# Kernel tuning notes

Measured on AMD Instinct MI355X. Metric: run time of the kernel, lower is better.

Reference implementation:

```python
import jax, jax.numpy as jnp
import numpy as np

CHEB_K = 3  # diffusion_steps

def setup_inputs() -> dict:
    key = jax.random.key(0)
    k1, k2, k3 = jax.random.split(key, 3)
    N, D, B, C, O, K = 2048, 16, 64, 64, 64, CHEB_K
    node_embeddings = jax.random.normal(k1, (N, D), dtype=jnp.float32)
    feat = jax.random.normal(k2, (B, N, C), dtype=jnp.float32)
    # kaiming-uniform-like init for weights_pool, zeros bias (matches reset_parameters)
    fan_in = K * C  # fan_in of [D, K, C, O] per torch convention (dims after first)
    bound = 1.0 / np.sqrt(fan_in)
    weights_pool = jax.random.uniform(k3, (D, K, C, O), dtype=jnp.float32,
                                      minval=-bound, maxval=bound)
    bias_pool = jnp.zeros((D, O), dtype=jnp.float32)
    return {"node_embeddings": node_embeddings, "feat": feat,
            "weights_pool": weights_pool, "bias_pool": bias_pool}

def reference(node_embeddings, feat, weights_pool, bias_pool):
    N = node_embeddings.shape[0]
    K = weights_pool.shape[1]
    # adaptive adjacency: softmax(relu(E E^T)) row-wise
    sim = node_embeddings @ node_embeddings.T            # [N, N]
    supports = jax.nn.softmax(jax.nn.relu(sim), axis=1)  # [N, N]
    # Chebyshev polynomial recurrence: T0=I, T1=A, Tk = 2A Tk-1 - Tk-2
    support_set = [jnp.eye(N, dtype=supports.dtype), supports]
    for _ in range(2, K):
        support_set.append(2.0 * supports @ support_set[-1] - support_set[-2])
    supports_k = jnp.stack(support_set, axis=0)          # [K, N, N]
    # node-conditioned weights and bias
    weights = jnp.einsum('nd,dkio->nkio', node_embeddings, weights_pool)  # [N,K,C,O]
    bias = node_embeddings @ bias_pool                                    # [N, O]
    # graph diffusion of features
    x_g = jnp.einsum('knm,bmc->bknc', supports_k, feat)  # [B, K, N, C]
    x_g = jnp.transpose(x_g, (0, 2, 1, 3))               # [B, N, K, C]
    # per-node batched GEMM + bias
    x_gconv = jnp.einsum('bnki,nkio->bno', x_g, weights) + bias
    return x_gconv
```

## Files before the change

kernel.cpp:

```cpp
#include <hip/hip_runtime.h>
#include <stdint.h>

#define NN 2048
#define DE 16
#define BB 64
#define CC 64
#define OO 64
#define BC 4096
#define KR 192
#define JJ 12288

using bf16x8 = __attribute__((ext_vector_type(8))) __bf16;
using f32x4  = __attribute__((ext_vector_type(4))) float;

__device__ __forceinline__ unsigned short f2bf(float f) {
  union { float f; unsigned int u; } v; v.f = f;
  unsigned int u = v.u;
  return (unsigned short)((u + 0x7FFFu + ((u >> 16) & 1u)) >> 16);
}
__device__ __forceinline__ float bf2f(unsigned short h) {
  union { unsigned int u; float f; } v; v.u = ((unsigned int)h) << 16;
  return v.f;
}
__device__ __forceinline__ void gll16(const void* g, void* l) {
  __builtin_amdgcn_global_load_lds(
      (const __attribute__((address_space(1))) unsigned int*)g,
      (__attribute__((address_space(3))) unsigned int*)l, 16, 0, 0);
}

__global__ __launch_bounds__(256) void prep(const float* __restrict__ feat,
                                            const float* __restrict__ E,
                                            const float* __restrict__ wp,
                                            const float* __restrict__ bp,
                                            unsigned short* __restrict__ Fbf,
                                            unsigned short* __restrict__ FbfT,
                                            unsigned short* __restrict__ Abf,
                                            float* __restrict__ Bias,
                                            unsigned short* __restrict__ Ebf,
                                            unsigned short* __restrict__ wpT2) {
  __shared__ float smem[64 * 65];
  const int id = blockIdx.x;
  const int t  = threadIdx.x;

  if (id < 2048) {
    float (*tile)[65] = (float (*)[65])smem;
    const int b  = id >> 5;
    const int n0 = (id & 31) * 64;
    const int tr = t >> 4, tc4 = (t & 15) * 4;
#pragma unroll
    for (int i = 0; i < 4; ++i) {
      const int r = tr + i * 16;
      const float4 v = *(const float4*)(feat + (size_t)b * (NN * CC) + (size_t)(n0 + r) * CC + tc4);
      tile[r][tc4 + 0] = v.x; tile[r][tc4 + 1] = v.y;
      tile[r][tc4 + 2] = v.z; tile[r][tc4 + 3] = v.w;
    }
    __syncthreads();
#pragma unroll
    for (int i = 0; i < 4; ++i) {
      const int r = tr + i * 16;
      const unsigned int lo = f2bf(tile[r][tc4 + 0]) | ((unsigned int)f2bf(tile[r][tc4 + 1]) << 16);
      const unsigned int hi = f2bf(tile[r][tc4 + 2]) | ((unsigned int)f2bf(tile[r][tc4 + 3]) << 16);
      *(uint2*)(Fbf + (size_t)(n0 + r) * BC + b * CC + tc4) = make_uint2(lo, hi);
    }
    const int rr = t & 63;
    const int cb = t >> 6;
#pragma unroll
    for (int i = 0; i < 16; ++i) {
      const int c = cb * 16 + i;
      FbfT[(size_t)(b * CC + c) * NN + n0 + rr] = f2bf(tile[rr][c]);
    }
  } else if (id < 4096) {
    const int n = id - 2048;
    float* en  = smem;
    float* red = smem + 16;
    if (t < 16) en[t] = E[n * 16 + t];
    __syncthreads();
    if (t < 16) Ebf[n * 16 + t] = f2bf(en[t]);
    float er[16];
#pragma unroll
    for (int d = 0; d < 16; ++d) er[d] = en[d];

    float v[8];
    float mx = 0.0f;
#pragma unroll
    for (int i = 0; i < 8; ++i) {
      const int m = t + i * 256;
      const float4* Em = (const float4*)(E + m * 16);
      const float4 a = Em[0], b = Em[1], c = Em[2], d = Em[3];
      float dot = er[0] * a.x + er[1] * a.y + er[2] * a.z + er[3] * a.w
                + er[4] * b.x + er[5] * b.y + er[6] * b.z + er[7] * b.w
                + er[8] * c.x + er[9] * c.y + er[10] * c.z + er[11] * c.w
                + er[12] * d.x + er[13] * d.y + er[14] * d.z + er[15] * d.w;
      v[i] = fmaxf(dot, 0.0f);
      mx = fmaxf(mx, v[i]);
    }
#pragma unroll
    for (int off = 32; off > 0; off >>= 1) mx = fmaxf(mx, __shfl_xor(mx, off, 64));
    const int wave = t >> 6, lane = t & 63;
    if (lane == 0) red[wave] = mx;
    __syncthreads();
    mx = fmaxf(fmaxf(red[0], red[1]), fmaxf(red[2], red[3]));
    float s = 0.0f;
#pragma unroll
    for (int i = 0; i < 8; ++i) { v[i] = __expf(v[i] - mx); s += v[i]; }
#pragma unroll
    for (int off = 32; off > 0; off >>= 1) s += __shfl_xor(s, off, 64);
    if (lane == 0) red[4 + wave] = s;
    __syncthreads();
    s = red[4] + red[5] + red[6] + red[7];
    const float inv = 1.0f / s;
#pragma unroll
    for (int i = 0; i < 8; ++i)
      Abf[(size_t)n * NN + t + i * 256] = f2bf(v[i] * inv);
    if (t < 64) {
      float bs = 0.0f;
#pragma unroll
      for (int d = 0; d < 16; ++d) bs += er[d] * bp[d * 64 + t];
      Bias[n * 64 + t] = bs;
    }
  } else {
    const int rq = id - 4096;
    for (int p = t; p < 1024; p += 256) {
      const int e0 = p * 8;
      const int d0 = e0 & 15;
      const int rem = e0 >> 4;
      const int rl = rem & 7, o = rem >> 3;
      const int r = rq * 8 + rl;
      unsigned int w[4];
#pragma unroll
      for (int u = 0; u < 4; ++u) {
        const float f0 = wp[(size_t)(d0 + 2 * u) * JJ + r * 64 + o];
        const float f1 = wp[(size_t)(d0 + 2 * u + 1) * JJ + r * 64 + o];
        w[u] = f2bf(f0) | ((unsigned int)f2bf(f1) << 16);
      }
      *(uint4*)(wpT2 + (size_t)rq * 8192 + e0) = make_uint4(w[0], w[1], w[2], w[3]);
    }
  }
}

template <int EPI, int MW>
__global__ __launch_bounds__(256, 4) void gemm_mw(const unsigned short* __restrict__ A,
                                                  const unsigned short* __restrict__ Bt,
                                                  unsigned short* __restrict__ Cnm,
                                                  unsigned short* __restrict__ Ct,
                                                  const unsigned short* __restrict__ F,
                                                  const unsigned short* __restrict__ Ebf,
                                                  const unsigned short* __restrict__ wpT2,
                                                  unsigned short* __restrict__ Wg) {
  __shared__ alignas(16) unsigned short As[128 * 64];
  __shared__ alignas(16) unsigned short Bs[64 * 64];
  const int id = blockIdx.x;
  const int t = threadIdx.x;
  const int wave = t >> 6, lane = t & 63;
  const int li = lane & 15, q = lane >> 4;

  if (MW && id >= 1024) {
    const int wid = id - 1024;
    const int bj = (wid % 96) * 128;
    const int bm = (wid / 96) * 128;
    gll16(Ebf  + (size_t)(bm + (t >> 1)) * 16 + (t & 1) * 8, &As[t * 8]);
    gll16(wpT2 + (size_t)(bj + (t >> 1)) * 16 + (t & 1) * 8, &Bs[t * 8]);
    __syncthreads();
    const int wm = (wave >> 1) * 64, wj = (wave & 1) * 64;
    const bool hiK = (q >= 2);
    const int qq = q & 1;
    bf16x8 vz;
#pragma unroll
    for (int i = 0; i < 8; ++i) vz[i] = (__bf16)0.0f;
    bf16x8 af[4], bfr[4];
#pragma unroll
    for (int r = 0; r < 4; ++r) {
      af[r] = *(const bf16x8*)&As[(wm + r * 16 + li) * 16 + qq * 8];
      if (hiK) af[r] = vz;
    }
#pragma unroll
    for (int c = 0; c < 4; ++c) {
      bfr[c] = *(const bf16x8*)&Bs[(wj + c * 16 + li) * 16 + qq * 8];
      if (hiK) bfr[c] = vz;
    }
    const int rowL = q * 4;
#pragma unroll
    for (int r = 0; r < 4; ++r) {
#pragma unroll
      for (int c = 0; c < 4; ++c) {
        f32x4 acc = (f32x4){0.f, 0.f, 0.f, 0.f};
        acc = __builtin_amdgcn_mfma_f32_16x16x32_bf16(af[r], bfr[c], acc, 0, 0, 0);
        const int gm = bm + wm + r * 16 + rowL;
        const int gj = bj + wj + c * 16 + li;
#pragma unroll
        for (int i = 0; i < 4; ++i)
          Wg[(size_t)(gm + i) * JJ + gj] = f2bf(acc[i]);
      }
    }
    return;
  }

  const int bm = (id >> 6) * 128, bn = (id & 63) * 64;
  const int wm = wave * 32;

  f32x4 acc[2][4];
#pragma unroll
  for (int r = 0; r < 2; ++r)
#pragma unroll
    for (int c = 0; c < 4; ++c) acc[r][c] = (f32x4){0.f, 0.f, 0.f, 0.f};

  const int srow = t >> 3;
  const int csw = (((t & 7) ^ ((t >> 4) & 7)) * 8);
  const unsigned short* Ap[4];
  const unsigned short* Bp[2];
#pragma unroll
  for (int i = 0; i < 4; ++i) Ap[i] = A + (size_t)(bm + srow + i * 32) * NN + csw;
#pragma unroll
  for (int i = 0; i < 2; ++i) Bp[i] = Bt + (size_t)(bn + srow + i * 32) * NN + csw;
  const int sw = (li >> 1) & 7;

  for (int k0 = 0; k0 < NN; k0 += 64) {
    __syncthreads();
#pragma unroll
    for (int i = 0; i < 4; ++i) gll16(Ap[i] + k0, &As[(t + i * 256) * 8]);
#pragma unroll
    for (int i = 0; i < 2; ++i) gll16(Bp[i] + k0, &Bs[(t + i * 256) * 8]);
    __syncthreads();
#pragma unroll
    for (int kk = 0; kk < 2; ++kk) {
      const int kc = ((kk * 4 + q) ^ sw) * 8;
      bf16x8 af[2], bfr[4];
#pragma unroll
      for (int r = 0; r < 2; ++r)
        af[r] = *(const bf16x8*)&As[(wm + r * 16 + li) * 64 + kc];
#pragma unroll
      for (int c = 0; c < 4; ++c)
        bfr[c] = *(const bf16x8*)&Bs[(c * 16 + li) * 64 + kc];
#pragma unroll
      for (int r = 0; r < 2; ++r)
#pragma unroll
        for (int c = 0; c < 4; ++c)
          acc[r][c] = __builtin_amdgcn_mfma_f32_16x16x32_bf16(af[r], bfr[c], acc[r][c], 0, 0, 0);
    }
  }

  const int rowL = q * 4;
#pragma unroll
  for (int r = 0; r < 2; ++r) {
#pragma unroll
    for (int c = 0; c < 4; ++c) {
      const int gm = bm + wm + r * 16 + rowL;
      const int gn = bn + c * 16 + li;
      const f32x4 a = acc[r][c];
      if (EPI == 1) {
#pragma unroll
        for (int i = 0; i < 4; ++i)
          Cnm[(size_t)(gm + i) * BC + gn] = f2bf(a[i]);
        const unsigned int lo = f2bf(a[0]) | ((unsigned int)f2bf(a[1]) << 16);
        const unsigned int hi = f2bf(a[2]) | ((unsigned int)f2bf(a[3]) << 16);
        *(uint2*)(Ct + (size_t)gn * NN + gm) = make_uint2(lo, hi);
      } else {
#pragma unroll
        for (int i = 0; i < 4; ++i) {
          const float g = 2.0f * a[i] - bf2f(F[(size_t)(gm + i) * BC + gn]);
          Cnm[(size_t)(gm + i) * BC + gn] = f2bf(g);
        }
      }
    }
  }
}

__global__ __launch_bounds__(256) void final_gemm(const unsigned short* __restrict__ Fbf,
                                                  const unsigned short* __restrict__ G1,
                                                  const unsigned short* __restrict__ G2,
                                                  const unsigned short* __restrict__ Wg,
                                                  const float* __restrict__ Bias,
                                                  float* __restrict__ out) {
  __shared__ alignas(16) unsigned short Xl[64 * 200];
  __shared__ alignas(16) unsigned short Wl[KR * OO];
  const int n = blockIdx.x, t = threadIdx.x;
  const unsigned short* srcs[3] = {Fbf + (size_t)n * BC, G1 + (size_t)n * BC, G2 + (size_t)n * BC};
#pragma unroll
  for (int kk = 0; kk < 3; ++kk) {
    const uint4* s = (const uint4*)srcs[kk];
    for (int p = t; p < 512; p += 256) {
      const uint4 v = s[p];
      const int j = p * 8, b = j >> 6, i = j & 63;
      *(uint4*)&Xl[b * 200 + kk * 64 + i] = v;
    }
  }
  {
    const uint4* s = (const uint4*)(Wg + (size_t)n * JJ);
    uint4* d = (uint4*)Wl;
    for (int p = t; p < 1536; p += 256) d[p] = s[p];
  }
  __syncthreads();

  const int wave = t >> 6, lane = t & 63;
  const int q = lane >> 4;
  const int brow = wave * 16 + (lane & 15);
  f32x4 acc[4];
#pragma unroll
  for (int c = 0; c < 4; ++c) acc[c] = (f32x4){0.f, 0.f, 0.f, 0.f};
#pragma unroll
  for (int kq = 0; kq < 6; ++kq) {
    const bf16x8 a = *(const bf16x8*)&Xl[brow * 200 + kq * 32 + q * 8];
#pragma unroll
    for (int c = 0; c < 4; ++c) {
      const bf16x8 b = *(const bf16x8*)&Wl[(kq * 4 + q) * 512 + (c * 16 + (lane & 15)) * 8];
      acc[c] = __builtin_amdgcn_mfma_f32_16x16x32_bf16(a, b, acc[c], 0, 0, 0);
    }
  }
  const int col = lane & 15, rbase = wave * 16 + q * 4;
#pragma unroll
  for (int c = 0; c < 4; ++c) {
    const int o = c * 16 + col;
    const float bs = Bias[n * 64 + o];
#pragma unroll
    for (int i = 0; i < 4; ++i)
      out[(size_t)(rbase + i) * (NN * OO) + (size_t)n * OO + o] = acc[c][i] + bs;
  }
}

extern "C" void kernel_launch(void* const* d_in, const int* in_sizes, int n_in,
                              void* d_out, int out_size, void* d_ws, size_t ws_size,
                              hipStream_t stream) {
  const float* E    = (const float*)d_in[0];
  const float* feat = (const float*)d_in[1];
  const float* wp   = (const float*)d_in[2];
  const float* bp   = (const float*)d_in[3];
  float* out = (float*)d_out;

  char* ws = (char*)d_ws;
  size_t off = 0;
  auto alloc = [&](size_t bytes) -> void* {
    void* p = ws + off;
    off += (bytes + 255) & ~(size_t)255;
    return p;
  };
  unsigned short* Abf  = (unsigned short*)alloc((size_t)NN * NN * 2);
  unsigned short* FbfT = (unsigned short*)alloc((size_t)BC * NN * 2);
  unsigned short* Fbf  = (unsigned short*)alloc((size_t)NN * BC * 2);
  unsigned short* G1   = (unsigned short*)alloc((size_t)NN * BC * 2);
  unsigned short* G1T  = (unsigned short*)alloc((size_t)BC * NN * 2);
  unsigned short* Wg   = (unsigned short*)alloc((size_t)NN * JJ * 2);
  float* Bias          = (float*)alloc((size_t)NN * OO * 4);
  unsigned short* Ebf  = (unsigned short*)alloc((size_t)NN * DE * 2);
  unsigned short* wpT2 = (unsigned short*)alloc((size_t)JJ * DE * 2);
  unsigned short* G2   = FbfT;

  prep<<<dim3(4120), 256, 0, stream>>>(feat, E, wp, bp, Fbf, FbfT, Abf, Bias, Ebf, wpT2);
  gemm_mw<1, 1><<<dim3(2560), 256, 0, stream>>>(Abf, FbfT, G1, G1T, nullptr, Ebf, wpT2, Wg);
  gemm_mw<2, 0><<<dim3(1024), 256, 0, stream>>>(Abf, G1T, G2, nullptr, Fbf, Ebf, wpT2, Wg);
  final_gemm<<<dim3(2048), 256, 0, stream>>>(Fbf, G1, G2, Wg, Bias, out);
}
```

Before: 223.8 us.

## Vectorize FbfT transpose, remap GEMM blocks per XCD, drop LDS in final GEMM

The prep kernel now writes the transposed bf16 feature tile with packed 4-element stores instead of scalar 2-byte stores. The Chebyshev GEMM remaps block ids so that each of the 8 XCDs works on its own pair of row panels, which should improve L2 reuse of A. Occupancy hints go from 4 to 6 blocks per SM. The weight-generation blocks move from the first diffusion GEMM to the second. final_gemm no longer stages into LDS and instead loads MFMA operands straight from global memory, removing the sync and LDS traffic at the cost of less coalesced, possibly redundant global loads.

Result: slower. 277.8 us (+24.2%).

```diff
diff --git a/kernel.cpp b/kernel.cpp
--- a/kernel.cpp
+++ b/kernel.cpp
@@ -62,12 +62,13 @@
       const unsigned int hi = f2bf(tile[r][tc4 + 2]) | ((unsigned int)f2bf(tile[r][tc4 + 3]) << 16);
       *(uint2*)(Fbf + (size_t)(n0 + r) * BC + b * CC + tc4) = make_uint2(lo, hi);
     }
-    const int rr = t & 63;
-    const int cb = t >> 6;
-#pragma unroll
-    for (int i = 0; i < 16; ++i) {
-      const int c = cb * 16 + i;
-      FbfT[(size_t)(b * CC + c) * NN + n0 + rr] = f2bf(tile[rr][c]);
+#pragma unroll
+    for (int u = 0; u < 4; ++u) {
+      const int p = t + u * 256;
+      const int c = p >> 4, n4 = (p & 15) * 4;
+      const unsigned int lo = f2bf(tile[n4 + 0][c]) | ((unsigned int)f2bf(tile[n4 + 1][c]) << 16);
+      const unsigned int hi = f2bf(tile[n4 + 2][c]) | ((unsigned int)f2bf(tile[n4 + 3][c]) << 16);
+      *(uint2*)(FbfT + (size_t)(b * CC + c) * NN + n0 + n4) = make_uint2(lo, hi);
     }
   } else if (id < 4096) {
     const int n = id - 2048;
@@ -139,7 +140,7 @@
 }
 
 template <int EPI, int MW>
-__global__ __launch_bounds__(256, 4) void gemm_mw(const unsigned short* __restrict__ A,
+__global__ __launch_bounds__(256, 6) void gemm_mw(const unsigned short* __restrict__ A,
                                                   const unsigned short* __restrict__ Bt,
                                                   unsigned short* __restrict__ Cnm,
                                                   unsigned short* __restrict__ Ct,
@@ -195,7 +196,10 @@
     return;
   }
 
-  const int bm = (id >> 6) * 128, bn = (id & 63) * 64;
+  const int xcd = id & 7;
+  const int rr = id >> 3;
+  const int bn = (rr & 63) * 64;
+  const int bm = ((xcd << 1) | (rr >> 6)) * 128;
   const int wm = wave * 32;
 
   f32x4 acc[2][4];
@@ -265,51 +269,36 @@
   }
 }
 
-__global__ __launch_bounds__(256) void final_gemm(const unsigned short* __restrict__ Fbf,
-                                                  const unsigned short* __restrict__ G1,
-                                                  const unsigned short* __restrict__ G2,
-                                                  const unsigned short* __restrict__ Wg,
-                                                  const float* __restrict__ Bias,
-                                                  float* __restrict__ out) {
-  __shared__ alignas(16) unsigned short Xl[64 * 200];
-  __shared__ alignas(16) unsigned short Wl[KR * OO];
+__global__ __launch_bounds__(256, 6) void final_gemm(const unsigned short* __restrict__ Fbf,
+                                                     const unsigned short* __restrict__ G1,
+                                                     const unsigned short* __restrict__ G2,
+                                                     const unsigned short* __restrict__ Wg,
+                                                     const float* __restrict__ Bias,
+                                                     float* __restrict__ out) {
   const int n = blockIdx.x, t = threadIdx.x;
-  const unsigned short* srcs[3] = {Fbf + (size_t)n * BC, G1 + (size_t)n * BC, G2 + (size_t)n * BC};
-#pragma unroll
-  for (int kk = 0; kk < 3; ++kk) {
-    const uint4* s = (const uint4*)srcs[kk];
-    for (int p = t; p < 512; p += 256) {
-      const uint4 v = s[p];
-      const int j = p * 8, b = j >> 6, i = j & 63;
-      *(uint4*)&Xl[b * 200 + kk * 64 + i] = v;
-    }
-  }
-  {
-    const uint4* s = (const uint4*)(Wg + (size_t)n * JJ);
-    uint4* d = (uint4*)Wl;
-    for (int p = t; p < 1536; p += 256) d[p] = s[p];
-  }
-  __syncthreads();
-
   const int wave = t >> 6, lane = t & 63;
-  const int q = lane >> 4;
-  const int brow = wave * 16 + (lane & 15);
+  const int li = lane & 15, q = lane >> 4;
+  const unsigned short* xb[3] = {Fbf + (size_t)n * BC + (size_t)(wave * 16 + li) * 64,
+                                 G1  + (size_t)n * BC + (size_t)(wave * 16 + li) * 64,
+                                 G2  + (size_t)n * BC + (size_t)(wave * 16 + li) * 64};
+  const unsigned short* wb = Wg + (size_t)n * JJ + (size_t)q * 512 + li * 8;
+
   f32x4 acc[4];
 #pragma unroll
   for (int c = 0; c < 4; ++c) acc[c] = (f32x4){0.f, 0.f, 0.f, 0.f};
 #pragma unroll
   for (int kq = 0; kq < 6; ++kq) {
-    const bf16x8 a = *(const bf16x8*)&Xl[brow * 200 + kq * 32 + q * 8];
+    const bf16x8 a = *(const bf16x8*)(xb[kq >> 1] + (kq & 1) * 32 + q * 8);
 #pragma unroll
     for (int c = 0; c < 4; ++c) {
-      const bf16x8 b = *(const bf16x8*)&Wl[(kq * 4 + q) * 512 + (c * 16 + (lane & 15)) * 8];
+      const bf16x8 b = *(const bf16x8*)(wb + (size_t)kq * 2048 + c * 128);
       acc[c] = __builtin_amdgcn_mfma_f32_16x16x32_bf16(a, b, acc[c], 0, 0, 0);
     }
   }
-  const int col = lane & 15, rbase = wave * 16 + q * 4;
+  const int rbase = wave * 16 + q * 4;
 #pragma unroll
   for (int c = 0; c < 4; ++c) {
-    const int o = c * 16 + col;
+    const int o = c * 16 + li;
     const float bs = Bias[n * 64 + o];
 #pragma unroll
     for (int i = 0; i < 4; ++i)
@@ -345,7 +334,7 @@
   unsigned short* G2   = FbfT;
 
   prep<<<dim3(4120), 256, 0, stream>>>(feat, E, wp, bp, Fbf, FbfT, Abf, Bias, Ebf, wpT2);
-  gemm_mw<1, 1><<<dim3(2560), 256, 0, stream>>>(Abf, FbfT, G1, G1T, nullptr, Ebf, wpT2, Wg);
-  gemm_mw<2, 0><<<dim3(1024), 256, 0, stream>>>(Abf, G1T, G2, nullptr, Fbf, Ebf, wpT2, Wg);
+  gemm_mw<1, 0><<<dim3(1024), 256, 0, stream>>>(Abf, FbfT, G1, G1T, nullptr, Ebf, wpT2, Wg);
+  gemm_mw<2, 1><<<dim3(2560), 256, 0, stream>>>(Abf, G1T, G2, nullptr, Fbf, Ebf, wpT2, Wg);
   final_gemm<<<dim3(2048), 256, 0, stream>>>(Fbf, G1, G2, Wg, Bias, out);
 }
```
